# Kernel optimization log

Hardware: AMD Instinct MI355X
Metric: run time of the kernel (lower is better)

The kernel has to match this reference:

```python
import jax, jax.numpy as jnp
import numpy as np

N_NODES = 10000
N_EDGES = 160000
D = 512            # input_dim = hidden_size = output_dim
NUM_EXPERTS = 4
N_LAYERS = 2


def setup_inputs() -> dict:
    key = jax.random.key(0)
    k = jax.random.split(key, 7)
    x = jax.random.normal(k[0], (N_NODES, D), dtype=jnp.float32)
    edge_index = jax.random.randint(k[1], (2, N_EDGES), 0, N_NODES, dtype=jnp.int32)
    # Gating network (Linear D -> NUM_EXPERTS)
    gate_w = jax.random.normal(k[2], (D, NUM_EXPERTS), dtype=jnp.float32) * 0.05
    gate_b = jnp.zeros((NUM_EXPERTS,), dtype=jnp.float32)
    # Per-expert SAGEConv weights: lin_r (self/root) and lin_l (neighbor) + bias
    w_self = jax.random.normal(k[3], (NUM_EXPERTS, N_LAYERS, D, D), dtype=jnp.float32) * 0.05
    w_neigh = jax.random.normal(k[4], (NUM_EXPERTS, N_LAYERS, D, D), dtype=jnp.float32) * 0.05
    b_exp = jnp.zeros((NUM_EXPERTS, N_LAYERS, D), dtype=jnp.float32)
    return {"x": x, "edge_index": edge_index, "gate_w": gate_w, "gate_b": gate_b,
            "w_self": w_self, "w_neigh": w_neigh, "b_exp": b_exp, "top_k": 1}


def reference(x, edge_index, gate_w, gate_b, w_self, w_neigh, b_exp, top_k):
    n = x.shape[0]
    src, dst = edge_index[0], edge_index[1]
    # mean-aggregation normalization (PyG SAGEConv aggr='mean'); 0 for isolated nodes
    deg = jax.ops.segment_sum(jnp.ones_like(src, dtype=x.dtype), dst, num_segments=n)
    inv_deg = jnp.where(deg > 0, 1.0 / jnp.maximum(deg, 1.0), 0.0)[:, None]  # [N,1]

    # gating: softmax(Linear(x)) then top-k routing
    gate = jax.nn.softmax(x @ gate_w + gate_b, axis=-1)          # [N, E]
    top_vals, top_idx = jax.lax.top_k(gate, top_k)               # [N, k]

    def expert(ws, wn, b):  # ws, wn: [L, D, D]; b: [L, D]
        h = x
        for l in range(N_LAYERS):
            agg = jax.ops.segment_sum(h[src], dst, num_segments=n) * inv_deg
            # SAGEConv: lin_l(mean_neigh) + lin_r(x) + bias, then relu (norm='id', eval dropout)
            h = jax.nn.relu(agg @ wn[l] + h @ ws[l] + b[l])
        return h

    # dense all-expert compute (matches original module)
    outs = jax.vmap(expert)(w_self, w_neigh, b_exp)              # [E, N, D]
    outs = jnp.transpose(outs, (1, 0, 2))                        # [N, E, D]
    sel = jnp.take_along_axis(outs, top_idx[:, :, None], axis=1)  # [N, k, D]
    return jnp.sum(sel * top_vals[:, :, None], axis=1)           # [N, D]
```

## Files before the change

kernel.cpp:

```cpp
#include <hip/hip_runtime.h>
#include <hip/hip_bf16.h>
#include <cstdint>

#define N_NODES 10000
#define N_EDGES 160000
#define DIM 512
#define K1 1024
#define NEXP 4

typedef __bf16 bf16_t;
typedef bf16_t bf16x8 __attribute__((ext_vector_type(8)));
typedef float f32x4 __attribute__((ext_vector_type(4)));

#define AS1(p) ((__attribute__((address_space(1))) void*)(p))
#define AS3(p) ((__attribute__((address_space(3))) void*)(p))

#define VMW(N) asm volatile("s_waitcnt vmcnt(" #N ")" ::: "memory")
#define MFMA16(d, a_, b_) d = __builtin_amdgcn_mfma_f32_16x16x32_bf16(a_, b_, d, 0, 0, 0)

__global__ void zero_kernel(int* __restrict__ deg, int* __restrict__ ecnt) {
    int i = blockIdx.x * blockDim.x + threadIdx.x;
    if (i < N_NODES) deg[i] = 0;
    if (i < NEXP) ecnt[i] = 0;
}

__global__ void gate_kernel(const float* __restrict__ x,
                            const float* __restrict__ gw,
                            const float* __restrict__ gb,
                            int* __restrict__ top_idx,
                            float* __restrict__ top_val,
                            bf16_t* __restrict__ acat) {
    const int wave = threadIdx.x >> 6;
    const int lane = threadIdx.x & 63;
    const int node = blockIdx.x * 4 + wave;
    if (node >= N_NODES) return;
    const float4* x4 = (const float4*)(x + (size_t)node * DIM);
    const float4* gw4 = (const float4*)gw;
    float4 xa = x4[lane * 2];
    float4 xb = x4[lane * 2 + 1];
    float xv[8] = { xa.x, xa.y, xa.z, xa.w, xb.x, xb.y, xb.z, xb.w };
    float a0 = 0.f, a1 = 0.f, a2 = 0.f, a3 = 0.f;
    #pragma unroll
    for (int c = 0; c < 8; c++) {
        float4 g = gw4[lane * 8 + c];
        a0 += xv[c] * g.x; a1 += xv[c] * g.y; a2 += xv[c] * g.z; a3 += xv[c] * g.w;
    }
    bf16x8 o;
    #pragma unroll
    for (int c = 0; c < 8; c++) o[c] = (bf16_t)xv[c];
    *(bf16x8*)(acat + (size_t)node * K1 + DIM + lane * 8) = o;
    for (int off = 32; off > 0; off >>= 1) {
        a0 += __shfl_xor(a0, off);
        a1 += __shfl_xor(a1, off);
        a2 += __shfl_xor(a2, off);
        a3 += __shfl_xor(a3, off);
    }
    if (lane == 0) {
        float z[4] = { a0 + gb[0], a1 + gb[1], a2 + gb[2], a3 + gb[3] };
        int bi = 0; float bm = z[0];
        for (int e = 1; e < 4; e++) if (z[e] > bm) { bm = z[e]; bi = e; }
        float den = 0.f;
        for (int e = 0; e < 4; e++) den += expf(z[e] - bm);
        top_idx[node] = bi;
        top_val[node] = 1.0f / den;
    }
}

__global__ void bucket_kernel(const int* __restrict__ top_idx,
                              int* __restrict__ ecnt,
                              int* __restrict__ lists) {
    __shared__ int lcnt[NEXP];
    __shared__ int base[NEXP];
    const int tid = threadIdx.x;
    if (tid < NEXP) lcnt[tid] = 0;
    __syncthreads();
    const int node = blockIdx.x * 256 + tid;
    int e = 0, rank = 0;
    if (node < N_NODES) {
        e = top_idx[node];
        rank = atomicAdd(&lcnt[e], 1);
    }
    __syncthreads();
    if (tid < NEXP) base[tid] = atomicAdd(&ecnt[tid], lcnt[tid]);
    __syncthreads();
    if (node < N_NODES) lists[e * N_NODES + base[e] + rank] = node;
}

__global__ void deg_kernel(const int* __restrict__ dst, int* __restrict__ deg) {
    int i = blockIdx.x * blockDim.x + threadIdx.x;
    if (i < N_EDGES) atomicAdd(&deg[dst[i]], 1);
}

__global__ void scan_kernel(const int* __restrict__ deg,
                            int* __restrict__ offs,
                            int* __restrict__ cursor) {
    __shared__ int wsum[16];
    __shared__ int carrysh;
    const int tid = threadIdx.x;
    const int lane = tid & 63;
    const int wv = tid >> 6;
    if (tid == 0) carrysh = 0;
    __syncthreads();
    for (int base = 0; base < N_NODES; base += 1024) {
        int i = base + tid;
        int v = (i < N_NODES) ? deg[i] : 0;
        int s = v;
        #pragma unroll
        for (int off = 1; off < 64; off <<= 1) {
            int t = __shfl_up(s, off);
            if (lane >= off) s += t;
        }
        if (lane == 63) wsum[wv] = s;
        int carry = carrysh;
        __syncthreads();
        if (wv == 0) {
            int w = (lane < 16) ? wsum[lane] : 0;
            #pragma unroll
            for (int off = 1; off < 16; off <<= 1) {
                int t = __shfl_up(w, off);
                if (lane >= off) w += t;
            }
            if (lane < 16) wsum[lane] = w;
        }
        __syncthreads();
        int wbase = (wv > 0) ? wsum[wv - 1] : 0;
        int excl = carry + wbase + s - v;
        if (i < N_NODES) { offs[i] = excl; cursor[i] = excl; }
        int total = wsum[15];
        __syncthreads();
        if (tid == 0) carrysh = carry + total;
        __syncthreads();
    }
    if (tid == 0) offs[N_NODES] = carrysh;
}

__global__ void fill_kernel(const int* __restrict__ src, const int* __restrict__ dst,
                            int* __restrict__ cursor, int* __restrict__ csr) {
    int i = blockIdx.x * blockDim.x + threadIdx.x;
    if (i < N_EDGES) {
        int d = dst[i];
        int p = atomicAdd(&cursor[d], 1);
        csr[p] = src[i];
    }
}

__global__ void wtrans_kernel(const float* __restrict__ w_neigh,
                              const float* __restrict__ w_self,
                              bf16_t* __restrict__ Bt) {
    __shared__ float tile[32][33];
    const int m = blockIdx.z;
    const bool isSelf = m >= 8;
    const int el = m & 7;
    const float* W = (isSelf ? w_self : w_neigh) + (size_t)el * DIM * DIM;
    const int k0 = blockIdx.x * 32;
    const int n0 = blockIdx.y * 32;
    const int tx = threadIdx.x, ty = threadIdx.y;
    for (int r = ty; r < 32; r += 8)
        tile[r][tx] = W[(size_t)(k0 + r) * DIM + n0 + tx];
    __syncthreads();
    for (int r = ty; r < 32; r += 8) {
        int n = n0 + r;
        int k = k0 + tx;
        Bt[((size_t)el * DIM + n) * K1 + (isSelf ? DIM : 0) + k] = (bf16_t)tile[tx][r];
    }
}

__global__ void agg1_kernel(const int* __restrict__ offs, const int* __restrict__ csr,
                            bf16_t* __restrict__ acat) {
    const int wave = threadIdx.x >> 6;
    const int lane = threadIdx.x & 63;
    const int node = blockIdx.x * 4 + wave;
    if (node >= N_NODES) return;
    const int c0 = lane * 8;
    float s[8] = {0,0,0,0,0,0,0,0};
    int beg = offs[node];
    int end = offs[node + 1];
    int d = end - beg;
    int p = beg;
    for (; p + 8 <= end; p += 8) {
        bf16x8 v[8];
        #pragma unroll
        for (int q = 0; q < 8; q++) {
            int idx = csr[p + q];
            v[q] = *(const bf16x8*)(acat + (size_t)idx * K1 + DIM + c0);
        }
        #pragma unroll
        for (int q = 0; q < 8; q++)
            #pragma unroll
            for (int k = 0; k < 8; k++) s[k] += (float)v[q][k];
    }
    for (; p + 4 <= end; p += 4) {
        bf16x8 v[4];
        #pragma unroll
        for (int q = 0; q < 4; q++) {
            int idx = csr[p + q];
            v[q] = *(const bf16x8*)(acat + (size_t)idx * K1 + DIM + c0);
        }
        #pragma unroll
        for (int q = 0; q < 4; q++)
            #pragma unroll
            for (int k = 0; k < 8; k++) s[k] += (float)v[q][k];
    }
    for (; p < end; p++) {
        int idx = csr[p];
        bf16x8 v0 = *(const bf16x8*)(acat + (size_t)idx * K1 + DIM + c0);
        #pragma unroll
        for (int k = 0; k < 8; k++) s[k] += (float)v0[k];
    }
    float w = d > 0 ? 1.0f / (float)d : 0.0f;
    bf16x8 o;
    #pragma unroll
    for (int k = 0; k < 8; k++) o[k] = (bf16_t)(s[k] * w);
    *(bf16x8*)(acat + (size_t)node * K1 + c0) = o;
}

__global__ void agg2_kernel(const int* __restrict__ offs, const int* __restrict__ csr,
                            const int* __restrict__ top_idx,
                            const bf16_t* __restrict__ h1, bf16_t* __restrict__ acat) {
    const int wave = threadIdx.x >> 6;
    const int lane = threadIdx.x & 63;
    const int node = blockIdx.x * 4 + wave;
    if (node >= N_NODES) return;
    const int c0 = lane * 8;
    const bf16_t* hb = h1 + (size_t)top_idx[node] * N_NODES * DIM;
    float s[8] = {0,0,0,0,0,0,0,0};
    int beg = offs[node];
    int end = offs[node + 1];
    int d = end - beg;
    int p = beg;
    for (; p + 8 <= end; p += 8) {
        bf16x8 v[8];
        #pragma unroll
        for (int q = 0; q < 8; q++) {
            int idx = csr[p + q];
            v[q] = *(const bf16x8*)(hb + (size_t)idx * DIM + c0);
        }
        #pragma unroll
        for (int q = 0; q < 8; q++)
            #pragma unroll
            for (int k = 0; k < 8; k++) s[k] += (float)v[q][k];
    }
    for (; p + 4 <= end; p += 4) {
        bf16x8 v[4];
        #pragma unroll
        for (int q = 0; q < 4; q++) {
            int idx = csr[p + q];
            v[q] = *(const bf16x8*)(hb + (size_t)idx * DIM + c0);
        }
        #pragma unroll
        for (int q = 0; q < 4; q++)
            #pragma unroll
            for (int k = 0; k < 8; k++) s[k] += (float)v[q][k];
    }
    for (; p < end; p++) {
        int idx = csr[p];
        bf16x8 v0 = *(const bf16x8*)(hb + (size_t)idx * DIM + c0);
        #pragma unroll
        for (int k = 0; k < 8; k++) s[k] += (float)v0[k];
    }
    float w = d > 0 ? 1.0f / (float)d : 0.0f;
    bf16x8 o;
    #pragma unroll
    for (int k = 0; k < 8; k++) o[k] = (bf16_t)(s[k] * w);
    *(bf16x8*)(acat + (size_t)node * K1 + c0) = o;
    *(bf16x8*)(acat + (size_t)node * K1 + DIM + c0) = *(const bf16x8*)(hb + (size_t)node * DIM + c0);
}

__global__ __launch_bounds__(512, 2)
void gemm_l1_kernel(const bf16_t* __restrict__ A,
                    const bf16_t* __restrict__ Bt,
                    const float* __restrict__ bias_all,
                    bf16_t* __restrict__ h1) {
    const int b = blockIdx.x;
    const int xcd = b & 7;
    const int loc = b >> 3;
    const int mtile = xcd * 2 + (loc >> 4);
    const int ntile = loc & 15;
    const int e = ntile >> 2;

    __shared__ __align__(16) bf16_t As[3 * 640 * 32];
    __shared__ __align__(16) bf16_t Bs[3 * 128 * 32];

    const int t = threadIdx.x;
    const int lane = t & 63;
    const int wave = t >> 6;
    const int rloc = t >> 2;
    const int cgl = ((t & 3) - ((t >> 3) & 3)) & 3;

    const bf16_t* pA0 = A + (size_t)min(mtile * 640 +   0 + rloc, N_NODES - 1) * K1 + cgl * 8;
    const bf16_t* pA1 = A + (size_t)min(mtile * 640 + 128 + rloc, N_NODES - 1) * K1 + cgl * 8;
    const bf16_t* pA2 = A + (size_t)min(mtile * 640 + 256 + rloc, N_NODES - 1) * K1 + cgl * 8;
    const bf16_t* pA3 = A + (size_t)min(mtile * 640 + 384 + rloc, N_NODES - 1) * K1 + cgl * 8;
    const bf16_t* pA4 = A + (size_t)min(mtile * 640 + 512 + rloc, N_NODES - 1) * K1 + cgl * 8;
    const bf16_t* pB0 = Bt + ((size_t)(e * 2 + 0) * DIM + (ntile & 3) * 128 + rloc) * K1 + cgl * 8;

    char* asb = (char*)&As[0];
    char* bsb = (char*)&Bs[0];

    auto stage_full = [&](int bu) {
        char* ab = asb + bu * 40960 + wave * 1024;
        char* bb = bsb + bu * 8192  + wave * 1024;
        __builtin_amdgcn_global_load_lds(AS1(pA0), AS3(ab),          16, 0, 0);
        __builtin_amdgcn_global_load_lds(AS1(pA1), AS3(ab + 8192),   16, 0, 0);
        __builtin_amdgcn_global_load_lds(AS1(pA2), AS3(ab + 16384),  16, 0, 0);
        __builtin_amdgcn_global_load_lds(AS1(pA3), AS3(ab + 24576),  16, 0, 0);
        __builtin_amdgcn_global_load_lds(AS1(pA4), AS3(ab + 32768),  16, 0, 0);
        __builtin_amdgcn_global_load_lds(AS1(pB0), AS3(bb),          16, 0, 0);
        pA0 += 32; pA1 += 32; pA2 += 32; pA3 += 32; pA4 += 32; pB0 += 32;
    };

    const int rfr = lane & 15;
    const int cpr = lane >> 4;
    const int wm = wave >> 1;
    const int wn = wave & 1;
    const int arow = wm * 160 + rfr;
    const int brow = wn * 64 + rfr;
    const int ppA = (cpr + (arow >> 1)) & 3;
    const int ppB = (cpr + (brow >> 1)) & 3;
    const int aoff = arow * 32 + ppA * 8;
    const int boff = brow * 32 + ppB * 8;

    f32x4 acc[10][4] = {};

    auto compute_full = [&](int bu) {
        const bf16_t* Ab = As + bu * 20480 + aoff;
        const bf16_t* Bb = Bs + bu * 4096  + boff;
        bf16x8 bfr[4];
        #pragma unroll
        for (int j = 0; j < 4; j++) bfr[j] = *(const bf16x8*)(Bb + j * 512);
        #pragma unroll
        for (int i = 0; i < 10; i++) {
            bf16x8 af = *(const bf16x8*)(Ab + i * 512);
            #pragma unroll
            for (int j = 0; j < 4; j++)
                MFMA16(acc[i][j], af, bfr[j]);
        }
    };

    stage_full(0);
    stage_full(1);

    int cb = 0, sb = 2;
    for (int tt = 0; tt < 31; ++tt) {
        VMW(6);
        __builtin_amdgcn_s_barrier();
        asm volatile("" ::: "memory");
        const bool st = (tt < 30);
        char* ab = asb + sb * 40960 + wave * 1024;
        char* bb = bsb + sb * 8192  + wave * 1024;
        const bf16_t* Ab = As + cb * 20480 + aoff;
        const bf16_t* Bb = Bs + cb * 4096  + boff;

        bf16x8 bq[4], aq[4];

        #pragma unroll
        for (int j = 0; j < 4; j++) bq[j] = *(const bf16x8*)(Bb + j * 512);
        #pragma unroll
        for (int i = 0; i < 4; i++) aq[i] = *(const bf16x8*)(Ab + i * 512);
        if (st) {
            __builtin_amdgcn_global_load_lds(AS1(pA0), AS3(ab),        16, 0, 0);
            __builtin_amdgcn_global_load_lds(AS1(pA1), AS3(ab + 8192), 16, 0, 0);
        }
        __builtin_amdgcn_s_barrier();
        asm volatile("s_waitcnt lgkmcnt(0)" ::: "memory");
        __builtin_amdgcn_sched_barrier(0);
        __builtin_amdgcn_s_setprio(1);
        #pragma unroll
        for (int i = 0; i < 4; i++)
            #pragma unroll
            for (int j = 0; j < 4; j++)
                MFMA16(acc[i][j], aq[i], bq[j]);
        __builtin_amdgcn_s_setprio(0);
        __builtin_amdgcn_s_barrier();

        #pragma unroll
        for (int i = 0; i < 3; i++) aq[i] = *(const bf16x8*)(Ab + (4 + i) * 512);
        if (st) {
            __builtin_amdgcn_global_load_lds(AS1(pA2), AS3(ab + 16384), 16, 0, 0);
            __builtin_amdgcn_global_load_lds(AS1(pA3), AS3(ab + 24576), 16, 0, 0);
        }
        __builtin_amdgcn_s_barrier();
        asm volatile("s_waitcnt lgkmcnt(0)" ::: "memory");
        __builtin_amdgcn_sched_barrier(0);
        __builtin_amdgcn_s_setprio(1);
        #pragma unroll
        for (int i = 0; i < 3; i++)
            #pragma unroll
            for (int j = 0; j < 4; j++)
                MFMA16(acc[4 + i][j], aq[i], bq[j]);
        __builtin_amdgcn_s_setprio(0);
        __builtin_amdgcn_s_barrier();

        #pragma unroll
        for (int i = 0; i < 3; i++) aq[i] = *(const bf16x8*)(Ab + (7 + i) * 512);
        if (st) {
            __builtin_amdgcn_global_load_lds(AS1(pA4), AS3(ab + 32768), 16, 0, 0);
            __builtin_amdgcn_global_load_lds(AS1(pB0), AS3(bb),         16, 0, 0);
        }
        __builtin_amdgcn_s_barrier();
        asm volatile("s_waitcnt lgkmcnt(0)" ::: "memory");
        __builtin_amdgcn_sched_barrier(0);
        __builtin_amdgcn_s_setprio(1);
        #pragma unroll
        for (int i = 0; i < 3; i++)
            #pragma unroll
            for (int j = 0; j < 4; j++)
                MFMA16(acc[7 + i][j], aq[i], bq[j]);
        __builtin_amdgcn_s_setprio(0);
        __builtin_amdgcn_s_barrier();

        if (st) {
            pA0 += 32; pA1 += 32; pA2 += 32; pA3 += 32; pA4 += 32; pB0 += 32;
            sb = (sb == 2) ? 0 : sb + 1;
        }
        cb = (cb == 2) ? 0 : cb + 1;
    }
    VMW(0);
    __builtin_amdgcn_s_barrier();
    asm volatile("" ::: "memory");
    compute_full(cb);

    const float* bias = bias_all + e * 1024;
    const int cobase = (ntile & 3) * 128 + wn * 64 + (lane & 15);
    float bv[4];
    #pragma unroll
    for (int j = 0; j < 4; j++) bv[j] = bias[cobase + j * 16];
    const int rbase = mtile * 640 + wm * 160 + (lane >> 4) * 4;
    #pragma unroll
    for (int i = 0; i < 10; i++) {
        #pragma unroll
        for (int r = 0; r < 4; r++) {
            int row = rbase + i * 16 + r;
            if (row < N_NODES) {
                bf16_t* cp = h1 + ((size_t)e * N_NODES + row) * DIM + cobase;
                #pragma unroll
                for (int j = 0; j < 4; j++) {
                    float v = fmaxf(acc[i][j][r] + bv[j], 0.f);
                    cp[j * 16] = (bf16_t)v;
                }
            }
        }
    }
}

template <int MODE>
__global__ __launch_bounds__(256)
void gemm_kernel(const bf16_t* __restrict__ A,
                 const bf16_t* __restrict__ Bt,
                 const int layer,
                 const float* __restrict__ bias_all,
                 bf16_t* __restrict__ h1,
                 float* __restrict__ out,
                 const int* __restrict__ lists,
                 const int* __restrict__ ecnt,
                 const float* __restrict__ top_val) {
    int bx, by, e;
    if (MODE == 0) {
        const int b = blockIdx.x;
        const int kq = b & 7;
        const int ke = kq >> 2;
        const int ky = kq & 3;
        const int r = b >> 3;
        const int yloc = r >> 3;
        const int xz = r & 7;
        bx = xz & 3;
        e = ke * 2 + (xz >> 2);
        by = ky * 20 + yloc;
        if (by >= 79) return;
    } else {
        bx = blockIdx.x; by = blockIdx.y; e = blockIdx.z;
    }
    int cnt = N_NODES;
    if (MODE == 1) {
        cnt = ecnt[e];
        if (by * 128 >= cnt) return;
    }
    __shared__ __align__(16) bf16_t As[128 * 32];
    __shared__ __align__(16) bf16_t Bs[128 * 32];

    const int t = threadIdx.x;
    const int lane = t & 63;
    const int wave = t >> 6;
    const int wm = wave >> 1;
    const int wn = wave & 1;

    const int r0 = t >> 2;
    const int rot = (t >> 3) & 3;
    const int cgl = ((t & 3) - rot) & 3;

    int i0 = by * 128 + r0;
    int i1 = i0 + 64;
    int arow0, arow1;
    if (MODE == 0) {
        arow0 = min(i0, N_NODES - 1);
        arow1 = min(i1, N_NODES - 1);
    } else {
        arow0 = lists[e * N_NODES + min(i0, cnt - 1)];
        arow1 = lists[e * N_NODES + min(i1, cnt - 1)];
    }
    const bf16_t* Bte = Bt + (size_t)(e * 2 + layer) * DIM * K1;
    const bf16_t* aptr0 = A + (size_t)arow0 * K1 + cgl * 8;
    const bf16_t* aptr1 = A + (size_t)arow1 * K1 + cgl * 8;
    const bf16_t* bptr0 = Bte + (size_t)(bx * 128 + r0) * K1 + cgl * 8;
    const bf16_t* bptr1 = bptr0 + (size_t)64 * K1;

    f32x4 acc[4][4] = {};
    char* asb = (char*)&As[0];
    char* bsb = (char*)&Bs[0];
    const int wb = wave * 1024;

    const int cpr = lane >> 4;
    const int rfr = lane & 15;

    for (int k0 = 0; k0 < K1; k0 += 32) {
        __syncthreads();
        __builtin_amdgcn_global_load_lds(AS1(aptr0), AS3(asb + wb),        16, 0, 0);
        __builtin_amdgcn_global_load_lds(AS1(aptr1), AS3(asb + 4096 + wb), 16, 0, 0);
        __builtin_amdgcn_global_load_lds(AS1(bptr0), AS3(bsb + wb),        16, 0, 0);
        __builtin_amdgcn_global_load_lds(AS1(bptr1), AS3(bsb + 4096 + wb), 16, 0, 0);
        __syncthreads();
        bf16x8 af[4], bfr[4];
        #pragma unroll
        for (int i = 0; i < 4; i++) {
            int r_full = wm * 64 + i * 16 + rfr;
            int p = (cpr + (r_full >> 1)) & 3;
            af[i] = *(const bf16x8*)(As + r_full * 32 + p * 8);
        }
        #pragma unroll
        for (int j = 0; j < 4; j++) {
            int r_full = wn * 64 + j * 16 + rfr;
            int p = (cpr + (r_full >> 1)) & 3;
            bfr[j] = *(const bf16x8*)(Bs + r_full * 32 + p * 8);
        }
        #pragma unroll
        for (int i = 0; i < 4; i++)
            #pragma unroll
            for (int j = 0; j < 4; j++)
                acc[i][j] = __builtin_amdgcn_mfma_f32_16x16x32_bf16(af[i], bfr[j], acc[i][j], 0, 0, 0);
        aptr0 += 32; aptr1 += 32; bptr0 += 32; bptr1 += 32;
    }

    const float* bias = bias_all + e * 1024 + layer * DIM;
    const int cbase = bx * 128 + wn * 64 + (lane & 15);
    float bv[4];
    #pragma unroll
    for (int j = 0; j < 4; j++) bv[j] = bias[cbase + j * 16];
    #pragma unroll
    for (int i = 0; i < 4; i++) {
        #pragma unroll
        for (int r = 0; r < 4; r++) {
            int row = by * 128 + wm * 64 + i * 16 + (lane >> 4) * 4 + r;
            if (MODE == 0) {
                if (row < N_NODES) {
                    bf16_t* cp = h1 + ((size_t)e * N_NODES + row) * DIM + cbase;
                    #pragma unroll
                    for (int j = 0; j < 4; j++) {
                        float v = fmaxf(acc[i][j][r] + bv[j], 0.f);
                        cp[j * 16] = (bf16_t)v;
                    }
                }
            } else {
                if (row < cnt) {
                    int node = lists[e * N_NODES + row];
                    float tv = top_val[node];
                    float* cp = out + (size_t)node * DIM + cbase;
                    #pragma unroll
                    for (int j = 0; j < 4; j++) {
                        float v = fmaxf(acc[i][j][r] + bv[j], 0.f);
                        cp[j * 16] = v * tv;
                    }
                }
            }
        }
    }
}

extern "C" void kernel_launch(void* const* d_in, const int* in_sizes, int n_in,
                              void* d_out, int out_size, void* d_ws, size_t ws_size,
                              hipStream_t stream) {
    const float* x       = (const float*)d_in[0];
    const int*   edge    = (const int*)d_in[1];
    const float* gw      = (const float*)d_in[2];
    const float* gb      = (const float*)d_in[3];
    const float* w_self  = (const float*)d_in[4];
    const float* w_neigh = (const float*)d_in[5];
    const float* b_exp   = (const float*)d_in[6];
    float* out = (float*)d_out;

    char* p = (char*)d_ws;
    auto alloc = [&](size_t bytes) {
        char* r = p;
        p += (bytes + 255) & ~(size_t)255;
        return r;
    };
    bf16_t* Bt      = (bf16_t*)alloc((size_t)8 * DIM * K1 * 2);
    bf16_t* acat    = (bf16_t*)alloc((size_t)N_NODES * K1 * 2);
    bf16_t* h1      = (bf16_t*)alloc((size_t)NEXP * N_NODES * DIM * 2);
    int*    deg     = (int*)alloc((size_t)N_NODES * 4);
    int*    offs    = (int*)alloc((size_t)(N_NODES + 1) * 4);
    int*    cursor  = (int*)alloc((size_t)N_NODES * 4);
    int*    csr     = (int*)alloc((size_t)N_EDGES * 4);
    int*    top_idx = (int*)alloc((size_t)N_NODES * 4);
    float*  top_val = (float*)alloc((size_t)N_NODES * 4);
    int*    ecnt    = (int*)alloc(256);
    int*    lists   = (int*)alloc((size_t)NEXP * N_NODES * 4);

    const int* srcE = edge;
    const int* dstE = edge + N_EDGES;

    zero_kernel<<<40, 256, 0, stream>>>(deg, ecnt);
    gate_kernel<<<N_NODES / 4, 256, 0, stream>>>(x, gw, gb, top_idx, top_val, acat);
    bucket_kernel<<<40, 256, 0, stream>>>(top_idx, ecnt, lists);
    deg_kernel<<<N_EDGES / 256, 256, 0, stream>>>(dstE, deg);
    scan_kernel<<<1, 1024, 0, stream>>>(deg, offs, cursor);
    fill_kernel<<<N_EDGES / 256, 256, 0, stream>>>(srcE, dstE, cursor, csr);
    wtrans_kernel<<<dim3(16, 16, 16), dim3(32, 8), 0, stream>>>(w_neigh, w_self, Bt);
    agg1_kernel<<<N_NODES / 4, 256, 0, stream>>>(offs, csr, acat);
    gemm_l1_kernel<<<256, 512, 0, stream>>>(acat, Bt, b_exp, h1);
    agg2_kernel<<<N_NODES / 4, 256, 0, stream>>>(offs, csr, top_idx, h1, acat);
    gemm_kernel<1><<<dim3(4, 79, 4), 256, 0, stream>>>(acat, Bt, 1, b_exp, nullptr, out, lists, ecnt, top_val);
}
```

Before: 273.0 us.

## Compact layer-2 routed GEMM into persistent grid over prefix-summed expert tiles

Adds a tiny kernel that prefix-sums the per-expert row-tile counts into a job table. The layer-2 routed GEMM is replaced by a 320-block grid-stride kernel that walks only the real (expert, row-tile, column-tile) jobs. Previously a 4x79x4 grid was launched and most blocks exited early because each expert holds only about a quarter of the nodes. This removes empty-block launch overhead and spreads work evenly across CUs, at the cost of one extra serial launch and a job lookup per tile.

```diff
diff --git a/kernel.cpp b/kernel.cpp
--- a/kernel.cpp
+++ b/kernel.cpp
@@ -86,6 +86,17 @@
     if (node < N_NODES) lists[e * N_NODES + base[e] + rank] = node;
 }
 
+__global__ void jobs_kernel(const int* __restrict__ ecnt, int* __restrict__ jobs) {
+    if (threadIdx.x == 0 && blockIdx.x == 0) {
+        int pref = 0;
+        for (int e = 0; e < NEXP; e++) {
+            jobs[e] = pref;
+            pref += (ecnt[e] + 127) >> 7;
+        }
+        jobs[4] = pref;
+    }
+}
+
 __global__ void deg_kernel(const int* __restrict__ dst, int* __restrict__ deg) {
     int i = blockIdx.x * blockDim.x + threadIdx.x;
     if (i < N_EDGES) atomicAdd(&deg[dst[i]], 1);
@@ -443,38 +454,15 @@
     }
 }
 
-template <int MODE>
 __global__ __launch_bounds__(256)
-void gemm_kernel(const bf16_t* __restrict__ A,
-                 const bf16_t* __restrict__ Bt,
-                 const int layer,
-                 const float* __restrict__ bias_all,
-                 bf16_t* __restrict__ h1,
-                 float* __restrict__ out,
-                 const int* __restrict__ lists,
-                 const int* __restrict__ ecnt,
-                 const float* __restrict__ top_val) {
-    int bx, by, e;
-    if (MODE == 0) {
-        const int b = blockIdx.x;
-        const int kq = b & 7;
-        const int ke = kq >> 2;
-        const int ky = kq & 3;
-        const int r = b >> 3;
-        const int yloc = r >> 3;
-        const int xz = r & 7;
-        bx = xz & 3;
-        e = ke * 2 + (xz >> 2);
-        by = ky * 20 + yloc;
-        if (by >= 79) return;
-    } else {
-        bx = blockIdx.x; by = blockIdx.y; e = blockIdx.z;
-    }
-    int cnt = N_NODES;
-    if (MODE == 1) {
-        cnt = ecnt[e];
-        if (by * 128 >= cnt) return;
-    }
+void gemm2_kernel(const bf16_t* __restrict__ A,
+                  const bf16_t* __restrict__ Bt,
+                  const float* __restrict__ bias_all,
+                  float* __restrict__ out,
+                  const int* __restrict__ lists,
+                  const int* __restrict__ ecnt,
+                  const int* __restrict__ jobs,
+                  const float* __restrict__ top_val) {
     __shared__ __align__(16) bf16_t As[128 * 32];
     __shared__ __align__(16) bf16_t Bs[128 * 32];
 
@@ -483,91 +471,82 @@
     const int wave = t >> 6;
     const int wm = wave >> 1;
     const int wn = wave & 1;
-
     const int r0 = t >> 2;
     const int rot = (t >> 3) & 3;
     const int cgl = ((t & 3) - rot) & 3;
-
-    int i0 = by * 128 + r0;
-    int i1 = i0 + 64;
-    int arow0, arow1;
-    if (MODE == 0) {
-        arow0 = min(i0, N_NODES - 1);
-        arow1 = min(i1, N_NODES - 1);
-    } else {
-        arow0 = lists[e * N_NODES + min(i0, cnt - 1)];
-        arow1 = lists[e * N_NODES + min(i1, cnt - 1)];
-    }
-    const bf16_t* Bte = Bt + (size_t)(e * 2 + layer) * DIM * K1;
-    const bf16_t* aptr0 = A + (size_t)arow0 * K1 + cgl * 8;
-    const bf16_t* aptr1 = A + (size_t)arow1 * K1 + cgl * 8;
-    const bf16_t* bptr0 = Bte + (size_t)(bx * 128 + r0) * K1 + cgl * 8;
-    const bf16_t* bptr1 = bptr0 + (size_t)64 * K1;
-
-    f32x4 acc[4][4] = {};
+    const int cpr = lane >> 4;
+    const int rfr = lane & 15;
     char* asb = (char*)&As[0];
     char* bsb = (char*)&Bs[0];
     const int wb = wave * 1024;
 
-    const int cpr = lane >> 4;
-    const int rfr = lane & 15;
-
-    for (int k0 = 0; k0 < K1; k0 += 32) {
-        __syncthreads();
-        __builtin_amdgcn_global_load_lds(AS1(aptr0), AS3(asb + wb),        16, 0, 0);
-        __builtin_amdgcn_global_load_lds(AS1(aptr1), AS3(asb + 4096 + wb), 16, 0, 0);
-        __builtin_amdgcn_global_load_lds(AS1(bptr0), AS3(bsb + wb),        16, 0, 0);
-        __builtin_amdgcn_global_load_lds(AS1(bptr1), AS3(bsb + 4096 + wb), 16, 0, 0);
-        __syncthreads();
-        bf16x8 af[4], bfr[4];
+    const int total = jobs[4] * 4;
+
+    for (int j = blockIdx.x; j < total; j += gridDim.x) {
+        const int byt = j >> 2;
+        const int bx = j & 3;
+        const int e = (byt >= jobs[1]) + (byt >= jobs[2]) + (byt >= jobs[3]);
+        const int by = byt - jobs[e];
+        const int cnt = ecnt[e];
+
+        int i0 = by * 128 + r0;
+        int i1 = i0 + 64;
+        int arow0 = lists[e * N_NODES + min(i0, cnt - 1)];
+        int arow1 = lists[e * N_NODES + min(i1, cnt - 1)];
+        const bf16_t* Bte = Bt + (size_t)(e * 2 + 1) * DIM * K1;
+        const bf16_t* aptr0 = A + (size_t)arow0 * K1 + cgl * 8;
+        const bf16_t* aptr1 = A + (size_t)arow1 * K1 + cgl * 8;
+        const bf16_t* bptr0 = Bte + (size_t)(bx * 128 + r0) * K1 + cgl * 8;
+        const bf16_t* bptr1 = bptr0 + (size_t)64 * K1;
+
+        f32x4 acc[4][4] = {};
+
+        for (int k0 = 0; k0 < K1; k0 += 32) {
+            __syncthreads();
+            __builtin_amdgcn_global_load_lds(AS1(aptr0), AS3(asb + wb),        16, 0, 0);
+            __builtin_amdgcn_global_load_lds(AS1(aptr1), AS3(asb + 4096 + wb), 16, 0, 0);
+            __builtin_amdgcn_global_load_lds(AS1(bptr0), AS3(bsb + wb),        16, 0, 0);
+            __builtin_amdgcn_global_load_lds(AS1(bptr1), AS3(bsb + 4096 + wb), 16, 0, 0);
+            __syncthreads();
+            bf16x8 af[4], bfr[4];
+            #pragma unroll
+            for (int i = 0; i < 4; i++) {
+                int r_full = wm * 64 + i * 16 + rfr;
+                int p = (cpr + (r_full >> 1)) & 3;
+                af[i] = *(const bf16x8*)(As + r_full * 32 + p * 8);
+            }
+            #pragma unroll
+            for (int jj = 0; jj < 4; jj++) {
+                int r_full = wn * 64 + jj * 16 + rfr;
+                int p = (cpr + (r_full >> 1)) & 3;
+                bfr[jj] = *(const bf16x8*)(Bs + r_full * 32 + p * 8);
+            }
+            #pragma unroll
+            for (int i = 0; i < 4; i++)
+                #pragma unroll
+                for (int jj = 0; jj < 4; jj++)
+                    acc[i][jj] = __builtin_amdgcn_mfma_f32_16x16x32_bf16(af[i], bfr[jj], acc[i][jj], 0, 0, 0);
+            aptr0 += 32; aptr1 += 32; bptr0 += 32; bptr1 += 32;
+        }
+
+        const float* bias = bias_all + e * 1024 + DIM;
+        const int cbase = bx * 128 + wn * 64 + (lane & 15);
+        float bv[4];
+        #pragma unroll
+        for (int jj = 0; jj < 4; jj++) bv[jj] = bias[cbase + jj * 16];
         #pragma unroll
         for (int i = 0; i < 4; i++) {
-            int r_full = wm * 64 + i * 16 + rfr;
-            int p = (cpr + (r_full >> 1)) & 3;
-            af[i] = *(const bf16x8*)(As + r_full * 32 + p * 8);
-        }
-        #pragma unroll
-        for (int j = 0; j < 4; j++) {
-            int r_full = wn * 64 + j * 16 + rfr;
-            int p = (cpr + (r_full >> 1)) & 3;
-            bfr[j] = *(const bf16x8*)(Bs + r_full * 32 + p * 8);
-        }
-        #pragma unroll
-        for (int i = 0; i < 4; i++)
-            #pragma unroll
-            for (int j = 0; j < 4; j++)
-                acc[i][j] = __builtin_amdgcn_mfma_f32_16x16x32_bf16(af[i], bfr[j], acc[i][j], 0, 0, 0);
-        aptr0 += 32; aptr1 += 32; bptr0 += 32; bptr1 += 32;
-    }
-
-    const float* bias = bias_all + e * 1024 + layer * DIM;
-    const int cbase = bx * 128 + wn * 64 + (lane & 15);
-    float bv[4];
-    #pragma unroll
-    for (int j = 0; j < 4; j++) bv[j] = bias[cbase + j * 16];
-    #pragma unroll
-    for (int i = 0; i < 4; i++) {
-        #pragma unroll
-        for (int r = 0; r < 4; r++) {
-            int row = by * 128 + wm * 64 + i * 16 + (lane >> 4) * 4 + r;
-            if (MODE == 0) {
-                if (row < N_NODES) {
-                    bf16_t* cp = h1 + ((size_t)e * N_NODES + row) * DIM + cbase;
-                    #pragma unroll
-                    for (int j = 0; j < 4; j++) {
-                        float v = fmaxf(acc[i][j][r] + bv[j], 0.f);
-                        cp[j * 16] = (bf16_t)v;
-                    }
-                }
-            } else {
+            #pragma unroll
+            for (int r = 0; r < 4; r++) {
+                int row = by * 128 + wm * 64 + i * 16 + (lane >> 4) * 4 + r;
                 if (row < cnt) {
                     int node = lists[e * N_NODES + row];
                     float tv = top_val[node];
                     float* cp = out + (size_t)node * DIM + cbase;
                     #pragma unroll
-                    for (int j = 0; j < 4; j++) {
-                        float v = fmaxf(acc[i][j][r] + bv[j], 0.f);
-                        cp[j * 16] = v * tv;
+                    for (int jj = 0; jj < 4; jj++) {
+                        float v = fmaxf(acc[i][jj][r] + bv[jj], 0.f);
+                        cp[jj * 16] = v * tv;
                     }
                 }
             }
@@ -604,6 +583,7 @@
     float*  top_val = (float*)alloc((size_t)N_NODES * 4);
     int*    ecnt    = (int*)alloc(256);
     int*    lists   = (int*)alloc((size_t)NEXP * N_NODES * 4);
+    int*    jobs    = ecnt + 8;
 
     const int* srcE = edge;
     const int* dstE = edge + N_EDGES;
@@ -611,6 +591,7 @@
     zero_kernel<<<40, 256, 0, stream>>>(deg, ecnt);
     gate_kernel<<<N_NODES / 4, 256, 0, stream>>>(x, gw, gb, top_idx, top_val, acat);
     bucket_kernel<<<40, 256, 0, stream>>>(top_idx, ecnt, lists);
+    jobs_kernel<<<1, 1, 0, stream>>>(ecnt, jobs);
     deg_kernel<<<N_EDGES / 256, 256, 0, stream>>>(dstE, deg);
     scan_kernel<<<1, 1024, 0, stream>>>(deg, offs, cursor);
     fill_kernel<<<N_EDGES / 256, 256, 0, stream>>>(srcE, dstE, cursor, csr);
@@ -618,5 +599,5 @@
     agg1_kernel<<<N_NODES / 4, 256, 0, stream>>>(offs, csr, acat);
     gemm_l1_kernel<<<256, 512, 0, stream>>>(acat, Bt, b_exp, h1);
     agg2_kernel<<<N_NODES / 4, 256, 0, stream>>>(offs, csr, top_idx, h1, acat);
-    gemm_kernel<1><<<dim3(4, 79, 4), 256, 0, stream>>>(acat, Bt, 1, b_exp, nullptr, out, lists, ecnt, top_val);
-}
+    gemm2_kernel<<<320, 256, 0, stream>>>(acat, Bt, b_exp, out, lists, ecnt, jobs, top_val);
+}
```

Result: no change. 267.9 us (-1.9%).
